# Kernel tuning notes

Hardware: AMD Instinct MI355X
Metric: run time of the kernel (lower is better)

## Reference

```python
import jax, jax.numpy as jnp
from jax import lax
import numpy as np

TAU_R = 1.0
TAU_W = 5.0
W_MIN, W_MAX = 0.0, 0.05
N_MBON, N_FBN, N_DAN, N_KC = 20, 60, 20, 200
N_RECUR = N_MBON + N_FBN + N_DAN
B, T = 256, 61


def setup_inputs() -> dict:
    key = jax.random.key(0)
    ks = jax.random.split(key, 8)
    r_kc = jax.random.uniform(ks[0], (B, N_KC, T), dtype=jnp.float32)
    r_ext = jax.random.uniform(ks[1], (B, 2, T), dtype=jnp.float32)
    time = jnp.arange(T, dtype=jnp.float32) * 0.5  # dt = 0.5
    # KC->MBON plastic weights start at the max value (0.05), as in init
    W0_W = jax.random.uniform(ks[2], (B, N_MBON, N_KC), dtype=jnp.float32) * W_MAX
    W0_w = jax.random.uniform(ks[3], (B, N_MBON, N_KC), dtype=jnp.float32) * W_MAX
    sqrt2 = np.sqrt(2.0)
    W_mbon = jax.random.normal(ks[4], (N_RECUR, N_MBON)) * np.sqrt(1.0 / (sqrt2 * N_MBON))
    W_fbn = jax.random.normal(ks[5], (N_RECUR, N_FBN)) * np.sqrt(1.0 / (sqrt2 * N_FBN))
    W_dan = jax.random.normal(ks[6], (N_RECUR, N_DAN)) * np.sqrt(1.0 / (sqrt2 * N_DAN))
    W_recur = jnp.concatenate([W_mbon, W_fbn, W_dan], axis=1).astype(jnp.float32)
    W_ext = jax.random.normal(ks[7], (N_FBN, 2), dtype=jnp.float32)
    bias = jnp.full((N_RECUR,), 0.1, dtype=jnp.float32)
    W_readout = jax.random.normal(jax.random.fold_in(key, 99), (1, N_MBON), dtype=jnp.float32) / np.sqrt(N_MBON)
    return {"r_kc": r_kc, "r_ext": r_ext, "time": time, "n_batch": B,
            "W0_W": W0_W, "W0_w": W0_w, "W_recur": W_recur, "W_ext": W_ext,
            "bias": bias, "W_readout": W_readout}


def reference(r_kc, r_ext, time, n_batch, W0_W, W0_w, W_recur, W_ext, bias, W_readout):
    n_mbon, n_kc = W0_W.shape[1], W0_W.shape[2]
    n_fbn = W_ext.shape[0]
    n_recur = W_recur.shape[0]
    n_dan = n_recur - n_mbon - n_fbn
    nb = r_kc.shape[0]
    dt = time[1] - time[0]

    # initial state: FBN/DAN at 0.1, MBON at 0
    r_init = jnp.full((nb, n_recur), 0.1, dtype=r_kc.dtype).at[:, :n_mbon].set(0.0)
    # DAN->MBON weights are zeroed
    Wr = W_recur.at[:n_mbon, -n_dan:].set(0.0)
    rbk0 = r_kc[:, :, 0]            # KC eligibility trace
    rbd0 = r_init[:, -n_dan:]       # DAN eligibility trace
    readout0 = jnp.einsum('om,bm->bo', W_readout, r_init[:, :n_mbon]).squeeze(-1)
    zeros_dan = jnp.zeros((nb, n_dan), dtype=r_kc.dtype)

    def step(carry, xs):
        r, W, wt, rbk, rbd = carry
        rk_t, re_t = xs                                   # [B,n_kc], [B,n_ext]
        I_kc = jnp.einsum('bmk,bk->bm', W, rk_t)          # KC -> MBON via plastic W
        I_fbn = jnp.einsum('fe,be->bf', W_ext, re_t)      # context -> FBN
        I_tot = jnp.concatenate([I_kc, I_fbn, zeros_dan], axis=1)
        Wr_prod = jnp.einsum('sr,br->bs', Wr, r)
        dr = (-r + jax.nn.relu(Wr_prod + bias + I_tot)) / TAU_R
        r_new = r + dr * dt
        # plasticity update (uses the *new* DAN activity)
        rbk_new = rbk + (rk_t - rbk) * dt / TAU_W
        r_dan = r_new[:, -n_dan:]
        rbd_new = rbd + (r_dan - rbd) * dt / TAU_W
        dw = (jnp.einsum('bd,bk->bdk', rbd_new, rk_t)
              - jnp.einsum('bd,bk->bdk', r_dan, rbk_new))
        wt_new = wt + dw * dt
        W_new = jnp.clip(W + (-W + wt_new) / TAU_W * dt, W_MIN, W_MAX)
        ro = jnp.einsum('om,bm->bo', W_readout, r_new[:, :n_mbon]).squeeze(-1)
        return (r_new, W_new, wt_new, rbk_new, rbd_new), (r_new, W_new, wt_new, ro)

    xs = (jnp.moveaxis(r_kc, 2, 0)[:-1], jnp.moveaxis(r_ext, 2, 0)[:-1])
    carry0 = (r_init, W0_W, W0_w, rbk0, rbd0)
    _, (r_s, W_s, wt_s, ro_s) = lax.scan(step, carry0, xs)
    r_series = jnp.concatenate([r_init[None], r_s], axis=0)    # [T,B,n_recur]
    W_series = jnp.concatenate([W0_W[None], W_s], axis=0)      # [T,B,n_mbon,n_kc]
    wt_series = jnp.concatenate([W0_w[None], wt_s], axis=0)    # [T,B,n_mbon,n_kc]
    readout = jnp.concatenate([readout0[None], ro_s], axis=0)  # [T,B]
    return r_series, W_series, wt_series, readout
```

## Files before the change

### kernel.cpp

```cpp
#include <hip/hip_runtime.h>


#define NKC   200
#define NREC  100
#define TSTEP 61
#define NSTEP 60
#define WRSTR 108
#define PSTR  52
#define NTHR  512

__device__ __forceinline__ void bar_lds() {
    __builtin_amdgcn_sched_barrier(0);
    asm volatile("s_waitcnt lgkmcnt(0)");
    __builtin_amdgcn_s_barrier();
    __builtin_amdgcn_sched_barrier(0);
}

__global__ __launch_bounds__(NTHR, 1) void cond_rnn_kernel(
    const float* __restrict__ r_kc, const float* __restrict__ r_ext,
    const float* __restrict__ timev, const float* __restrict__ W0_W,
    const float* __restrict__ W0_w, const float* __restrict__ W_recur,
    const float* __restrict__ W_ext, const float* __restrict__ bias,
    const float* __restrict__ W_readout, float* __restrict__ out, int B)
{
    const int b   = blockIdx.x;
    const int tid = threadIdx.x;
    const float dt  = timev[1] - timev[0];
    const float dtw = dt / 5.0f;

    __shared__ __align__(16) float s_rk[TSTEP * NKC];
    __shared__ __align__(16) float s_re[128];
    __shared__ __align__(16) float s_Wr[NREC * WRSTR];
    __shared__ __align__(16) float s_Wro[32];
    __shared__ __align__(16) float s_r[2][112];
    __shared__ __align__(16) float s_rbd[32];
    __shared__ __align__(16) float s_part[20 * PSTR];

    const float* rk_b = r_kc + (size_t)b * (NKC * TSTEP);
    for (int f = tid; f < NKC * TSTEP; f += NTHR) {
        int k = f / TSTEP, t = f - k * TSTEP;
        s_rk[t * NKC + k] = rk_b[f];
    }
    const float* re_b = r_ext + (size_t)b * (2 * TSTEP);
    if (tid < 2 * TSTEP) s_re[tid] = re_b[tid];
    for (int f = tid; f < NREC * NREC; f += NTHR) {
        int s = f / NREC, j = f - s * NREC;
        float v = W_recur[f];
        if (s < 20 && j >= 80) v = 0.f;
        s_Wr[s * WRSTR + j] = v;
    }
    if (tid < 20)  s_Wro[tid] = W_readout[tid];
    if (tid < 100) s_r[0][tid] = (tid < 20) ? 0.f : 0.1f;
    if (tid < 20)  s_rbd[tid] = 0.1f;

    float my_bias = 0.f, we0 = 0.f, we1 = 0.f;
    if (tid < 100) my_bias = bias[tid];
    if (tid >= 20 && tid < 80) { we0 = W_ext[(tid - 20) * 2]; we1 = W_ext[(tid - 20) * 2 + 1]; }
    float rbd_mine = 0.1f;
    float r_mine   = (tid < 20) ? 0.f : 0.1f;

    float* out_r  = out;
    float* out_W  = out + (size_t)TSTEP * B * 100;
    float* out_wt = out_W + (size_t)TSTEP * B * 4000;
    float* out_ro = out_wt + (size_t)TSTEP * B * 4000;

    float4 Wreg[2], wtreg[2], rbkreg[2];
    const float* W0Wb = W0_W + (size_t)b * 4000;
    const float* W0wb = W0_w + (size_t)b * 4000;
    #pragma unroll
    for (int i = 0; i < 2; ++i) {
        int c = tid + NTHR * i;
        if (c < 1000) {
            Wreg[i]  = *(const float4*)(W0Wb + 4 * c);
            wtreg[i] = *(const float4*)(W0wb + 4 * c);
            *(float4*)(out_W  + (size_t)b * 4000 + 4 * c) = Wreg[i];
            *(float4*)(out_wt + (size_t)b * 4000 + 4 * c) = wtreg[i];
        }
    }
    if (tid < 100) out_r[(size_t)b * 100 + tid] = r_mine;

    __syncthreads();

    #pragma unroll
    for (int i = 0; i < 2; ++i) {
        int c = tid + NTHR * i;
        if (c < 1000) {
            int k0 = (4 * c) % NKC;
            int m  = c / 50;
            float4 rk0 = *(const float4*)(s_rk + k0);
            rbkreg[i] = rk0;
            float4 w = Wreg[i];
            s_part[m * PSTR + (c % 50)] =
                w.x * rk0.x + w.y * rk0.y + w.z * rk0.z + w.w * rk0.w;
        }
    }
    if (tid == 255) {
        float ro = 0.f;
        #pragma unroll
        for (int mm = 0; mm < 20; ++mm) ro += s_Wro[mm] * s_r[0][mm];
        out_ro[b] = ro;
    }
    __syncthreads();

    for (int it = 0; it < NSTEP; ++it) {
        const int cur = it & 1, nxt = cur ^ 1;

        if (tid < 100) {
            float acc = my_bias;
            if (tid < 20) {
                const float* pp = s_part + tid * PSTR;
                #pragma unroll
                for (int q4 = 0; q4 < 12; ++q4) {
                    float4 p4 = *(const float4*)(pp + 4 * q4);
                    acc += p4.x + p4.y + p4.z + p4.w;
                }
                acc += pp[48] + pp[49];
            } else if (tid < 80) {
                acc = fmaf(we0, s_re[it], acc);
                acc = fmaf(we1, s_re[TSTEP + it], acc);
            }
            const float* wr = s_Wr + tid * WRSTR;
            #pragma unroll
            for (int j4 = 0; j4 < 25; ++j4) {
                float4 w4 = *(const float4*)(wr + 4 * j4);
                float4 r4 = *(const float4*)(&s_r[cur][4 * j4]);
                acc = fmaf(w4.x, r4.x, acc); acc = fmaf(w4.y, r4.y, acc);
                acc = fmaf(w4.z, r4.z, acc); acc = fmaf(w4.w, r4.w, acc);
            }
            float drive = acc > 0.f ? acc : 0.f;
            float rn = r_mine + dt * (drive - r_mine);
            r_mine = rn;
            s_r[nxt][tid] = rn;
            out_r[(size_t)(it + 1) * B * 100 + (size_t)b * 100 + tid] = rn;
            if (tid >= 80) {
                rbd_mine += (rn - rbd_mine) * dtw;
                s_rbd[tid - 80] = rbd_mine;
            }
        }
        bar_lds();

        float* oW  = out_W  + (size_t)(it + 1) * B * 4000 + (size_t)b * 4000;
        float* owt = out_wt + (size_t)(it + 1) * B * 4000 + (size_t)b * 4000;
        const float* rk_cur = s_rk + it * NKC;
        const float* rk_nx  = s_rk + (it + 1) * NKC;
        #pragma unroll
        for (int i = 0; i < 2; ++i) {
            int c = tid + NTHR * i;
            if (c < 1000) {
                int k0 = (4 * c) % NKC;
                int m  = c / 50;
                float4 rk4 = *(const float4*)(rk_cur + k0);
                float4 rkn = *(const float4*)(rk_nx + k0);
                float rbdn = s_rbd[m];
                float rdan = s_r[nxt][80 + m];
                float4 rb = rbkreg[i];
                rb.x += (rk4.x - rb.x) * dtw;  rb.y += (rk4.y - rb.y) * dtw;
                rb.z += (rk4.z - rb.z) * dtw;  rb.w += (rk4.w - rb.w) * dtw;
                rbkreg[i] = rb;
                float4 wt = wtreg[i];
                wt.x = fmaf(rbdn * rk4.x - rdan * rb.x, dt, wt.x);
                wt.y = fmaf(rbdn * rk4.y - rdan * rb.y, dt, wt.y);
                wt.z = fmaf(rbdn * rk4.z - rdan * rb.z, dt, wt.z);
                wt.w = fmaf(rbdn * rk4.w - rdan * rb.w, dt, wt.w);
                wtreg[i] = wt;
                float4 w = Wreg[i];
                w.x += (wt.x - w.x) * dtw;  w.y += (wt.y - w.y) * dtw;
                w.z += (wt.z - w.z) * dtw;  w.w += (wt.w - w.w) * dtw;
                w.x = fminf(fmaxf(w.x, 0.f), 0.05f);
                w.y = fminf(fmaxf(w.y, 0.f), 0.05f);
                w.z = fminf(fmaxf(w.z, 0.f), 0.05f);
                w.w = fminf(fmaxf(w.w, 0.f), 0.05f);
                Wreg[i] = w;
                s_part[m * PSTR + (c % 50)] =
                    w.x * rkn.x + w.y * rkn.y + w.z * rkn.z + w.w * rkn.w;
                *(float4*)(owt + 4 * c) = wt;
                *(float4*)(oW  + 4 * c) = w;
            }
        }
        if (tid == 255) {
            float ro = 0.f;
            #pragma unroll
            for (int mm = 0; mm < 20; ++mm) ro += s_Wro[mm] * s_r[nxt][mm];
            out_ro[(size_t)(it + 1) * B + b] = ro;
        }
        bar_lds();
    }
}

extern "C" void kernel_launch(void* const* d_in, const int* in_sizes, int n_in,
                              void* d_out, int out_size, void* d_ws, size_t ws_size,
                              hipStream_t stream) {
    const float* r_kc      = (const float*)d_in[0];
    const float* r_ext     = (const float*)d_in[1];
    const float* timev     = (const float*)d_in[2];
    const float* W0_W      = (const float*)d_in[4];
    const float* W0_w      = (const float*)d_in[5];
    const float* W_recur   = (const float*)d_in[6];
    const float* W_ext     = (const float*)d_in[7];
    const float* bias      = (const float*)d_in[8];
    const float* W_readout = (const float*)d_in[9];

    const int B = in_sizes[0] / (NKC * TSTEP);
    cond_rnn_kernel<<<dim3(B), dim3(NTHR), 0, stream>>>(
        r_kc, r_ext, timev, W0_W, W0_w, W_recur, W_ext, bias, W_readout,
        (float*)d_out, B);
}
```

Measured before the change: 520.4 us.

## Use nontemporal output stores, remap blocks across XCDs, keep current rk in registers

All global output stores become nontemporal so the large streaming W and wt time series bypass cache retention. Block indices are remapped so consecutive batch elements land on the same XCD (8-way interleave), changing the L2 and memory locality of the output writes. The current-timestep KC rates are carried in registers from the previous iteration, removing one LDS float4 load per element each step. The remap is only applied when B is divisible by 8.

```diff
diff --git a/kernel.cpp b/kernel.cpp
--- a/kernel.cpp
+++ b/kernel.cpp
@@ -9,11 +9,22 @@
 #define PSTR  52
 #define NTHR  512
 
+typedef float vfloat4 __attribute__((ext_vector_type(4)));
+
 __device__ __forceinline__ void bar_lds() {
     __builtin_amdgcn_sched_barrier(0);
     asm volatile("s_waitcnt lgkmcnt(0)");
     __builtin_amdgcn_s_barrier();
     __builtin_amdgcn_sched_barrier(0);
+}
+
+__device__ __forceinline__ void nt_store4(float* p, float4 v) {
+    vfloat4 t;
+    t.x = v.x; t.y = v.y; t.z = v.z; t.w = v.w;
+    __builtin_nontemporal_store(t, (vfloat4*)p);
+}
+__device__ __forceinline__ void nt_store1(float* p, float v) {
+    __builtin_nontemporal_store(v, p);
 }
 
 __global__ __launch_bounds__(NTHR, 1) void cond_rnn_kernel(
@@ -23,7 +34,11 @@
     const float* __restrict__ W_ext, const float* __restrict__ bias,
     const float* __restrict__ W_readout, float* __restrict__ out, int B)
 {
-    const int b   = blockIdx.x;
+    int b = blockIdx.x;
+    if ((B & 7) == 0) {
+        const int cpx = B >> 3;
+        b = (blockIdx.x & 7) * cpx + (blockIdx.x >> 3);
+    }
     const int tid = threadIdx.x;
     const float dt  = timev[1] - timev[0];
     const float dtw = dt / 5.0f;
@@ -64,7 +79,7 @@
     float* out_wt = out_W + (size_t)TSTEP * B * 4000;
     float* out_ro = out_wt + (size_t)TSTEP * B * 4000;
 
-    float4 Wreg[2], wtreg[2], rbkreg[2];
+    float4 Wreg[2], wtreg[2], rbkreg[2], rkc[2];
     const float* W0Wb = W0_W + (size_t)b * 4000;
     const float* W0wb = W0_w + (size_t)b * 4000;
     #pragma unroll
@@ -73,11 +88,11 @@
         if (c < 1000) {
             Wreg[i]  = *(const float4*)(W0Wb + 4 * c);
             wtreg[i] = *(const float4*)(W0wb + 4 * c);
-            *(float4*)(out_W  + (size_t)b * 4000 + 4 * c) = Wreg[i];
-            *(float4*)(out_wt + (size_t)b * 4000 + 4 * c) = wtreg[i];
-        }
-    }
-    if (tid < 100) out_r[(size_t)b * 100 + tid] = r_mine;
+            nt_store4(out_W  + (size_t)b * 4000 + 4 * c, Wreg[i]);
+            nt_store4(out_wt + (size_t)b * 4000 + 4 * c, wtreg[i]);
+        }
+    }
+    if (tid < 100) nt_store1(out_r + (size_t)b * 100 + tid, r_mine);
 
     __syncthreads();
 
@@ -89,6 +104,7 @@
             int m  = c / 50;
             float4 rk0 = *(const float4*)(s_rk + k0);
             rbkreg[i] = rk0;
+            rkc[i]    = rk0;
             float4 w = Wreg[i];
             s_part[m * PSTR + (c % 50)] =
                 w.x * rk0.x + w.y * rk0.y + w.z * rk0.z + w.w * rk0.w;
@@ -98,7 +114,7 @@
         float ro = 0.f;
         #pragma unroll
         for (int mm = 0; mm < 20; ++mm) ro += s_Wro[mm] * s_r[0][mm];
-        out_ro[b] = ro;
+        nt_store1(out_ro + b, ro);
     }
     __syncthreads();
 
@@ -131,7 +147,7 @@
             float rn = r_mine + dt * (drive - r_mine);
             r_mine = rn;
             s_r[nxt][tid] = rn;
-            out_r[(size_t)(it + 1) * B * 100 + (size_t)b * 100 + tid] = rn;
+            nt_store1(out_r + (size_t)(it + 1) * B * 100 + (size_t)b * 100 + tid, rn);
             if (tid >= 80) {
                 rbd_mine += (rn - rbd_mine) * dtw;
                 s_rbd[tid - 80] = rbd_mine;
@@ -141,7 +157,6 @@
 
         float* oW  = out_W  + (size_t)(it + 1) * B * 4000 + (size_t)b * 4000;
         float* owt = out_wt + (size_t)(it + 1) * B * 4000 + (size_t)b * 4000;
-        const float* rk_cur = s_rk + it * NKC;
         const float* rk_nx  = s_rk + (it + 1) * NKC;
         #pragma unroll
         for (int i = 0; i < 2; ++i) {
@@ -149,8 +164,9 @@
             if (c < 1000) {
                 int k0 = (4 * c) % NKC;
                 int m  = c / 50;
-                float4 rk4 = *(const float4*)(rk_cur + k0);
+                float4 rk4 = rkc[i];
                 float4 rkn = *(const float4*)(rk_nx + k0);
+                rkc[i] = rkn;
                 float rbdn = s_rbd[m];
                 float rdan = s_r[nxt][80 + m];
                 float4 rb = rbkreg[i];
@@ -173,15 +189,15 @@
                 Wreg[i] = w;
                 s_part[m * PSTR + (c % 50)] =
                     w.x * rkn.x + w.y * rkn.y + w.z * rkn.z + w.w * rkn.w;
-                *(float4*)(owt + 4 * c) = wt;
-                *(float4*)(oW  + 4 * c) = w;
+                nt_store4(owt + 4 * c, wt);
+                nt_store4(oW  + 4 * c, w);
             }
         }
         if (tid == 255) {
             float ro = 0.f;
             #pragma unroll
             for (int mm = 0; mm < 20; ++mm) ro += s_Wro[mm] * s_r[nxt][mm];
-            out_ro[(size_t)(it + 1) * B + b] = ro;
+            nt_store1(out_ro + (size_t)(it + 1) * B + b, ro);
         }
         bar_lds();
     }
```

Measured after the change: 520.4 us. Within noise of the previous version (+0.0%).
